# Performance work log

Hardware: AMD Instinct MI355X
Metric: run time of the kernel (lower is better)

The kernel has to match this reference:

```python
import jax, jax.numpy as jnp
import numpy as np

P_TOKENS = 200  # num_prompt_tokens
N_HEADS = 4


def setup_inputs() -> dict:
    key = jax.random.key(0)
    ks = jax.random.split(key, 6)
    B, N, C = 64, 1224, 1024
    D = 256  # bottleneck / down_size
    s = 0.02
    return {
        "x": jax.random.normal(ks[0], (B, N, C), dtype=jnp.float32),
        "down_W": jax.random.normal(ks[1], (D, C), dtype=jnp.float32) * s,
        "down_b": jnp.zeros((D,), jnp.float32),
        "up_W": jax.random.normal(ks[2], (C, D), dtype=jnp.float32) * s,
        "up_b": jnp.zeros((C,), jnp.float32),
        "in_proj_W": jax.random.normal(ks[3], (3 * D, D), dtype=jnp.float32) * s,
        "in_proj_b": jnp.zeros((3 * D,), jnp.float32),
        "out_proj_W": jax.random.normal(ks[4], (D, D), dtype=jnp.float32) * s,
        "out_proj_b": jnp.zeros((D,), jnp.float32),
        "gate": jnp.float32(1.0),
    }


def _forward(x, down_W, down_b, up_W, up_b, in_proj_W, in_proj_b,
             out_proj_W, out_proj_b, gate):
    B, N, C = x.shape
    E = down_W.shape[0]
    hd = E // N_HEADS
    # down projection + exact GELU (torch nn.GELU default)
    down = jax.nn.gelu(x @ down_W.T + down_b, approximate=False)  # [B,N,E]
    prompt = down[:, :P_TOKENS, :]   # [B,P,E]
    tok = down[:, P_TOKENS:, :]      # [B,T,E]
    # --- nn.MultiheadAttention(prompt, prompt, prompt) ---
    qkv = prompt @ in_proj_W.T + in_proj_b            # [B,P,3E]
    q, k, v = jnp.split(qkv, 3, axis=-1)
    def heads(t):
        return t.reshape(B, P_TOKENS, N_HEADS, hd)
    q, k, v = heads(q), heads(k), heads(v)
    attn = jnp.einsum('bqhd,bkhd->bhqk', q, k) / jnp.sqrt(jnp.float32(hd))
    attn = jax.nn.softmax(attn, axis=-1)
    sa = jnp.einsum('bhqk,bkhd->bqhd', attn, v).reshape(B, P_TOKENS, E)
    sa = sa @ out_proj_W.T + out_proj_b               # [B,P,E]
    # --- manual cross attention prompt -> tokens ---
    scale = jnp.float32(E) ** -0.5
    cross = jax.nn.softmax(jnp.einsum('bpe,bte->bpt', sa, tok) * scale, axis=-1)
    prompt_out = jnp.einsum('bpt,bte->bpe', cross, tok)  # [B,P,E]
    combined = jnp.concatenate([prompt_out, tok], axis=1)  # [B,N,E]
    up = combined @ up_W.T + up_b                          # [B,N,C]
    return gate * up


def reference(x, down_W, down_b, up_W, up_b, in_proj_W, in_proj_b,
              out_proj_W, out_proj_b, gate):
    return _forward(x, down_W, down_b, up_W, up_b, in_proj_W, in_proj_b,
                    out_proj_W, out_proj_b, gate)
```

## Files before the change

kernel.cpp:

```cpp
#include <hip/hip_runtime.h>
#include <math.h>

#define BB 64
#define NN 1224
#define CC 1024
#define DD 256
#define PP 200
#define TT 1024
#define HH 4
#define HDD 64

typedef __attribute__((ext_vector_type(8))) short bf16x8;
typedef __attribute__((ext_vector_type(4))) float f32x4;
typedef unsigned short u16;
typedef unsigned long long u64;

__device__ __forceinline__ u16 f2bf(float f) {
  union { float f; unsigned int u; } v; v.f = f;
  unsigned int r = v.u + 0x7FFF + ((v.u >> 16) & 1);
  return (u16)(r >> 16);
}
__device__ __forceinline__ float bf2f(u16 h) {
  union { unsigned int u; float f; } v; v.u = ((unsigned int)h) << 16;
  return v.f;
}
__device__ __forceinline__ unsigned int pk2(float a, float b) {
  return (unsigned int)f2bf(a) | ((unsigned int)f2bf(b) << 16);
}
__device__ __forceinline__ void gload16(const void* g, void* l) {
  __builtin_amdgcn_global_load_lds(
      (const __attribute__((address_space(1))) void*)g,
      (__attribute__((address_space(3))) void*)l, 16, 0, 0);
}
__device__ __forceinline__ f32x4 ntld4(const float* p) {
  return __builtin_nontemporal_load((const f32x4*)p);
}

static const size_t SZ_DOWN = (size_t)BB * NN * DD * 2;
static const size_t SZ_TOKT = (size_t)BB * DD * TT * 2;
static const size_t SZ_Q    = (size_t)BB * HH * PP * HDD * 2;
static const size_t SZ_SCORES = (size_t)BB * PP * TT * 2;

static const size_t B_DOWN   = 0;
static const size_t B_TOKT   = B_DOWN + SZ_DOWN;
static const size_t B_POOL   = B_TOKT + SZ_TOKT;
static const size_t B_QB     = B_POOL;
static const size_t B_KB     = B_QB + SZ_Q;
static const size_t B_VB     = B_KB + SZ_Q;
static const size_t B_SA     = B_VB + SZ_Q;
static const size_t B_SA2    = B_SA + SZ_Q;
static const size_t B_PBF    = B_POOL;
static const size_t B_POUTBF = B_SA2;
static const size_t B_SCORES = B_SA2 + SZ_Q;
static const size_t B_W      = B_SCORES + SZ_SCORES * 2;
static const size_t B_WD     = B_W;
static const size_t B_WU     = B_WD + 524288;
static const size_t B_WIP    = B_WU + 524288;
static const size_t B_WOP    = B_WIP + 393216;

#define MFMA_STEP64(Ab, Bb) \
  _Pragma("unroll") \
  for (int kk = 0; kk < 64; kk += 32) { \
    bf16x8 af[4], bfr[2]; \
    _Pragma("unroll") \
    for (int mi = 0; mi < 4; ++mi) { \
      const int R = mi * 16 + (lane & 15); \
      const int byt = (R * 128 + (kk + (lane >> 4) * 8) * 2) ^ ((R & 7) << 4); \
      af[mi] = *(const bf16x8*)((const char*)Ab + byt); \
    } \
    _Pragma("unroll") \
    for (int ni = 0; ni < 2; ++ni) { \
      const int R = wave * 32 + ni * 16 + (lane & 15); \
      const int byt = (R * 128 + (kk + (lane >> 4) * 8) * 2) ^ ((R & 7) << 4); \
      bfr[ni] = *(const bf16x8*)((const char*)Bb + byt); \
    } \
    _Pragma("unroll") \
    for (int mi = 0; mi < 4; ++mi) \
      _Pragma("unroll") \
      for (int ni = 0; ni < 2; ++ni) \
        acc[mi][ni] = __builtin_amdgcn_mfma_f32_16x16x32_bf16(af[mi], bfr[ni], acc[mi][ni], 0, 0, 0); \
  }

#define GLOAD_A1(Ab, SRC) \
  { \
    const int L = wave * 1024 + lane * 16; \
    const int r = L >> 7; \
    const int ce = ((L & 127) ^ ((r & 7) << 4)) >> 1; \
    gload16((SRC), (char*)Ab + wave * 1024); \
  }

#define GLOAD_B4(Bb, SRC) \
  _Pragma("unroll") \
  for (int ii = 0; ii < 4; ++ii) { \
    const int slot = wave * 4 + ii; \
    const int L = slot * 1024 + lane * 16; \
    const int r = L >> 7; \
    const int ce = ((L & 127) ^ ((r & 7) << 4)) >> 1; \
    gload16((SRC), (char*)Bb + slot * 1024); \
  }

#define PIPE_WAIT(N) asm volatile("s_waitcnt vmcnt(" #N ")" ::: "memory");
#define PIPE_BAR() \
  __builtin_amdgcn_s_barrier(); \
  __builtin_amdgcn_sched_barrier(0);
#define PIPE_END() \
  asm volatile("s_waitcnt lgkmcnt(0)" ::: "memory"); \
  __builtin_amdgcn_s_barrier(); \
  __builtin_amdgcn_sched_barrier(0);

__global__ __launch_bounds__(256) void k_castw(const float* __restrict__ dW,
                                               const float* __restrict__ uW,
                                               const float* __restrict__ iW,
                                               const float* __restrict__ oW,
                                               u16* __restrict__ dWb, u16* __restrict__ uWb,
                                               u16* __restrict__ iWb, u16* __restrict__ oWb)
{
  const int id = blockIdx.x * 256 + threadIdx.x;
  const float* s; u16* d; int off;
  if (id < 65536)       { s = dW; d = dWb; off = id; }
  else if (id < 131072) { s = uW; d = uWb; off = id - 65536; }
  else if (id < 180224) { s = iW; d = iWb; off = id - 131072; }
  else                  { s = oW; d = oWb; off = id - 180224; }
  const float4 v = ((const float4*)s)[off];
  uint2 p; p.x = pk2(v.x, v.y); p.y = pk2(v.z, v.w);
  *(uint2*)&d[(size_t)off * 4] = p;
}

__global__ __launch_bounds__(512) void k_down(const float* __restrict__ x,
                                              const u16* __restrict__ Wd,
                                              const float* __restrict__ bias,
                                              u16* __restrict__ out,
                                              u16* __restrict__ tokT)
{
  __shared__ u16 Ab[2][64 * 64];
  __shared__ u16 Bb[2][256 * 64];
  const int tid = threadIdx.x;
  const int lane = tid & 63, wave = tid >> 6;
  f32x4 acc[4][2] = {};
  const int m0 = blockIdx.x * 64;
  const int ar0 = tid >> 4;
  const int c4 = (tid & 15) * 4;

  f32x4 areg[2];
#pragma unroll
  for (int i = 0; i < 2; ++i)
    areg[i] = ntld4(&x[(size_t)(m0 + ar0 + 32 * i) * CC + c4]);
#pragma unroll
  for (int i = 0; i < 2; ++i) {
    const int r = ar0 + 32 * i;
    uint2 p; p.x = pk2(areg[i].x, areg[i].y); p.y = pk2(areg[i].z, areg[i].w);
    *(uint2*)((char*)Ab[0] + ((r * 128 + c4 * 2) ^ ((r & 7) << 4))) = p;
  }
  GLOAD_B4(Bb[0], &Wd[(size_t)r * CC + 0 + ce])
#pragma unroll
  for (int i = 0; i < 2; ++i)
    areg[i] = ntld4(&x[(size_t)(m0 + ar0 + 32 * i) * CC + 64 + c4]);

  for (int it = 0; it < 16; ++it) {
    const int cur = it & 1;
    if (it < 14) {
#pragma unroll
      for (int i = 0; i < 2; ++i) {
        const int r = ar0 + 32 * i;
        uint2 p; p.x = pk2(areg[i].x, areg[i].y); p.y = pk2(areg[i].z, areg[i].w);
        *(uint2*)((char*)Ab[cur ^ 1] + ((r * 128 + c4 * 2) ^ ((r & 7) << 4))) = p;
      }
      const int kx = (it + 2) * 64;
#pragma unroll
      for (int i = 0; i < 2; ++i)
        areg[i] = ntld4(&x[(size_t)(m0 + ar0 + 32 * i) * CC + kx + c4]);
      const int kb = (it + 1) * 64;
      GLOAD_B4(Bb[cur ^ 1], &Wd[(size_t)r * CC + kb + ce])
      asm volatile("s_waitcnt vmcnt(6) lgkmcnt(0)" ::: "memory");
    } else if (it == 14) {
#pragma unroll
      for (int i = 0; i < 2; ++i) {
        const int r = ar0 + 32 * i;
        uint2 p; p.x = pk2(areg[i].x, areg[i].y); p.y = pk2(areg[i].z, areg[i].w);
        *(uint2*)((char*)Ab[cur ^ 1] + ((r * 128 + c4 * 2) ^ ((r & 7) << 4))) = p;
      }
      GLOAD_B4(Bb[cur ^ 1], &Wd[(size_t)r * CC + 960 + ce])
      asm volatile("s_waitcnt vmcnt(4) lgkmcnt(0)" ::: "memory");
    } else {
      asm volatile("s_waitcnt vmcnt(0) lgkmcnt(0)" ::: "memory");
    }
    PIPE_BAR()
    MFMA_STEP64(Ab[cur], Bb[cur])
    PIPE_END()
  }
#pragma unroll
  for (int mi = 0; mi < 4; ++mi) {
#pragma unroll
    for (int ni = 0; ni < 2; ++ni) {
      const int col = wave * 32 + ni * 16 + (lane & 15);
      const float bv = bias[col];
      u16 vs[4];
#pragma unroll
      for (int r = 0; r < 4; ++r) {
        const int row = m0 + mi * 16 + (lane >> 4) * 4 + r;
        float v = acc[mi][ni][r] + bv;
        v = 0.5f * v * (1.f + erff(v * 0.7071067811865475f));
        vs[r] = f2bf(v);
        out[(size_t)row * DD + col] = vs[r];
      }
      const int row0 = m0 + mi * 16 + (lane >> 4) * 4;
      const int b = row0 / NN, rr = row0 - b * NN;
      if (rr >= PP) {
        const u64 pk = (u64)vs[0] | ((u64)vs[1] << 16) | ((u64)vs[2] << 32) | ((u64)vs[3] << 48);
        *(u64*)&tokT[((size_t)(b * DD + col)) * TT + (rr - PP)] = pk;
      }
    }
  }
}

__global__ __launch_bounds__(512) void k_qkv(const u16* __restrict__ down,
                                             const u16* __restrict__ Wip,
                                             const float* __restrict__ bias,
                                             u16* __restrict__ qb,
                                             u16* __restrict__ kb,
                                             u16* __restrict__ vb)
{
  __shared__ u16 Ab[2][64 * 64];
  __shared__ u16 Bb[2][256 * 64];
  const int tid = threadIdx.x;
  const int lane = tid & 63, wave = tid >> 6;
  f32x4 acc[4][2] = {};
  const int m0 = blockIdx.x * 64;
  const int nt = blockIdx.y;

#define QKV_A(BUF, K0) GLOAD_A1(BUF, ({ const int m = m0 + r; const int b = m / PP; const int p = m - b * PP; \
                    &down[((size_t)(b * NN + p)) * DD + (K0) + ce]; }))
  QKV_A(Ab[0], 0)
  GLOAD_B4(Bb[0], &Wip[(size_t)(nt * 256 + r) * DD + 0 + ce])
  for (int it = 0; it < 4; ++it) {
    const int cur = it & 1;
    if (it < 3) {
      const int k0 = (it + 1) * 64;
      QKV_A(Ab[cur ^ 1], k0)
      GLOAD_B4(Bb[cur ^ 1], &Wip[(size_t)(nt * 256 + r) * DD + k0 + ce])
      PIPE_WAIT(5)
    } else { PIPE_WAIT(0) }
    PIPE_BAR()
    MFMA_STEP64(Ab[cur], Bb[cur])
    PIPE_END()
  }
#undef QKV_A
  u16* dst = (nt == 0) ? qb : ((nt == 1) ? kb : vb);
#pragma unroll
  for (int mi = 0; mi < 4; ++mi) {
#pragma unroll
    for (int ni = 0; ni < 2; ++ni) {
      const int n = wave * 32 + ni * 16 + (lane & 15);
      const float bv = bias[nt * 256 + n];
      const int h = n >> 6, dd = n & 63;
#pragma unroll
      for (int r = 0; r < 4; ++r) {
        const int m = m0 + mi * 16 + (lane >> 4) * 4 + r;
        const int b = m / PP, p = m - b * PP;
        dst[(((size_t)(b * HH + h)) * PP + p) * HDD + dd] = f2bf(acc[mi][ni][r] + bv);
      }
    }
  }
}

__global__ __launch_bounds__(512) void k_attn(const u16* __restrict__ qb,
                                              const u16* __restrict__ kb,
                                              const u16* __restrict__ vb,
                                              u16* __restrict__ sa)
{
  __shared__ u16 Ks[208 * 64];
  __shared__ u16 Vt[64 * 232];
  __shared__ u16 Pb[8 * 16 * 232];
  const int tid = threadIdx.x, lane = tid & 63, wave = tid >> 6;
  const int bh = blockIdx.x;
  const size_t kvbase = (size_t)bh * (PP * HDD);

  for (int it = 0; it < 7; ++it) {
    const int idx = tid + 512 * it;
    if (idx < 3200) {
      const int e = idx * 4;
      const int j = e >> 6, d = e & 63;
      const u64 kv = *(const u64*)&kb[kvbase + e];
      const int byt = (j * 128 + d * 2) ^ ((j & 7) << 4);
      *(u64*)((char*)Ks + byt) = kv;
      const u64 vv = *(const u64*)&vb[kvbase + e];
      const u16* vp = (const u16*)&vv;
#pragma unroll
      for (int w = 0; w < 4; ++w) Vt[(d + w) * 232 + j] = vp[w];
    }
  }
  if (tid < 128) {
    const int rr = 200 + (tid >> 4), c = (tid & 15) * 4;
    const int byt = (rr * 128 + c * 2) ^ ((rr & 7) << 4);
    *(u64*)((char*)Ks + byt) = 0ULL;
  }
  {
    const int d = tid >> 3, cg = tid & 7;
    *(u64*)&Vt[d * 232 + 200 + cg * 4] = 0ULL;
  }
  {
    u16* pw = Pb + wave * (16 * 232);
#pragma unroll
    for (int w = 0; w < 2; ++w) {
      const int idx = lane + 64 * w;
      if (idx < 96) {
        const int row = idx / 6, cg = idx - row * 6;
        *(u64*)&pw[row * 232 + 208 + cg * 4] = 0ULL;
      }
    }
  }
  __syncthreads();

  const int b_ = bh >> 2, h = bh & 3;
  const u16* qbase = qb + kvbase;
  u16* pw = Pb + wave * (16 * 232);

  for (int f = wave; f < 13; f += 8) {
    int qrow = f * 16 + (lane & 15); if (qrow > 199) qrow = 199;
    bf16x8 qa[2];
#pragma unroll
    for (int kk = 0; kk < 2; ++kk)
      qa[kk] = *(const bf16x8*)&qbase[(size_t)qrow * 64 + kk * 32 + (lane >> 4) * 8];

    f32x4 s[13];
#pragma unroll
    for (int nf = 0; nf < 13; ++nf) {
      const int R = nf * 16 + (lane & 15);
      f32x4 a = {};
#pragma unroll
      for (int kk = 0; kk < 2; ++kk) {
        const int byt = (R * 128 + (kk * 32 + (lane >> 4) * 8) * 2) ^ ((R & 7) << 4);
        const bf16x8 kf = *(const bf16x8*)((const char*)Ks + byt);
        a = __builtin_amdgcn_mfma_f32_16x16x32_bf16(qa[kk], kf, a, 0, 0, 0);
      }
      s[nf] = a;
    }
    float mx[4] = {-1e30f, -1e30f, -1e30f, -1e30f};
#pragma unroll
    for (int nf = 0; nf < 13; ++nf) {
      const int col = nf * 16 + (lane & 15);
#pragma unroll
      for (int r = 0; r < 4; ++r) {
        float v = (col < PP) ? s[nf][r] * 0.125f : -INFINITY;
        s[nf][r] = v;
        mx[r] = fmaxf(mx[r], v);
      }
    }
#pragma unroll
    for (int off = 1; off < 16; off <<= 1)
#pragma unroll
      for (int r = 0; r < 4; ++r) mx[r] = fmaxf(mx[r], __shfl_xor(mx[r], off));
    float sum[4] = {0.f, 0.f, 0.f, 0.f};
#pragma unroll
    for (int nf = 0; nf < 13; ++nf)
#pragma unroll
      for (int r = 0; r < 4; ++r) {
        const float e = expf(s[nf][r] - mx[r]);
        s[nf][r] = e;
        sum[r] += e;
      }
#pragma unroll
    for (int off = 1; off < 16; off <<= 1)
#pragma unroll
      for (int r = 0; r < 4; ++r) sum[r] += __shfl_xor(sum[r], off);
    float inv[4];
#pragma unroll
    for (int r = 0; r < 4; ++r) inv[r] = 1.f / sum[r];
#pragma unroll
    for (int nf = 0; nf < 13; ++nf) {
      const int col = nf * 16 + (lane & 15);
#pragma unroll
      for (int r = 0; r < 4; ++r) {
        const int row = (lane >> 4) * 4 + r;
        pw[row * 232 + col] = f2bf(s[nf][r] * inv[r]);
      }
    }
    f32x4 o[4] = {};
#pragma unroll
    for (int kk = 0; kk < 7; ++kk) {
      const bf16x8 pa = *(const bf16x8*)((const char*)pw +
                         ((lane & 15) * 232 + kk * 32 + (lane >> 4) * 8) * 2);
#pragma unroll
      for (int nf4 = 0; nf4 < 4; ++nf4) {
        const bf16x8 vv = *(const bf16x8*)((const char*)Vt +
                           (((lane & 15) + 16 * nf4) * 232 + kk * 32 + (lane >> 4) * 8) * 2);
        o[nf4] = __builtin_amdgcn_mfma_f32_16x16x32_bf16(pa, vv, o[nf4], 0, 0, 0);
      }
    }
#pragma unroll
    for (int nf4 = 0; nf4 < 4; ++nf4) {
      const int d = (lane & 15) + 16 * nf4;
#pragma unroll
      for (int r = 0; r < 4; ++r) {
        const int p = f * 16 + (lane >> 4) * 4 + r;
        if (p < PP)
          sa[((size_t)(b_ * PP + p)) * DD + h * HDD + d] = f2bf(o[nf4][r]);
      }
    }
  }
}

__global__ __launch_bounds__(512) void k_oproj(const u16* __restrict__ A,
                                               const u16* __restrict__ Wop,
                                               const float* __restrict__ bias,
                                               u16* __restrict__ out)
{
  __shared__ u16 Ab[2][64 * 64];
  __shared__ u16 Bb[2][256 * 64];
  const int tid = threadIdx.x;
  const int lane = tid & 63, wave = tid >> 6;
  f32x4 acc[4][2] = {};
  const int m0 = blockIdx.x * 64;

  GLOAD_A1(Ab[0], &A[(size_t)(m0 + r) * DD + 0 + ce])
  GLOAD_B4(Bb[0], &Wop[(size_t)r * DD + 0 + ce])
  for (int it = 0; it < 4; ++it) {
    const int cur = it & 1;
    if (it < 3) {
      const int k0 = (it + 1) * 64;
      GLOAD_A1(Ab[cur ^ 1], &A[(size_t)(m0 + r) * DD + k0 + ce])
      GLOAD_B4(Bb[cur ^ 1], &Wop[(size_t)r * DD + k0 + ce])
      PIPE_WAIT(5)
    } else { PIPE_WAIT(0) }
    PIPE_BAR()
    MFMA_STEP64(Ab[cur], Bb[cur])
    PIPE_END()
  }
#pragma unroll
  for (int mi = 0; mi < 4; ++mi) {
#pragma unroll
    for (int ni = 0; ni < 2; ++ni) {
      const int col = wave * 32 + ni * 16 + (lane & 15);
      const float bv = bias[col];
#pragma unroll
      for (int r = 0; r < 4; ++r) {
        const int row = m0 + mi * 16 + (lane >> 4) * 4 + r;
        out[(size_t)row * DD + col] = f2bf(acc[mi][ni][r] + bv);
      }
    }
  }
}

__global__ __launch_bounds__(512) void k_scores(const u16* __restrict__ sa2,
                                                const u16* __restrict__ down,
                                                u16* __restrict__ scores)
{
  __shared__ u16 Ab[2][64 * 64];
  __shared__ u16 Bb[2][256 * 64];
  const int tid = threadIdx.x;
  const int lane = tid & 63, wave = tid >> 6;
  f32x4 acc[4][2] = {};
  const int b = blockIdx.x, mh = blockIdx.y, nt = blockIdx.z;

#define SC_A(BUF, K0) GLOAD_A1(BUF, ({ int p = mh * 64 + r; p = (p < PP) ? p : (PP - 1); \
                    &sa2[((size_t)(b * PP + p)) * DD + (K0) + ce]; }))
  SC_A(Ab[0], 0)
  GLOAD_B4(Bb[0], &down[((size_t)(b * NN + PP + nt * 256 + r)) * DD + 0 + ce])
  for (int it = 0; it < 4; ++it) {
    const int cur = it & 1;
    if (it < 3) {
      const int k0 = (it + 1) * 64;
      SC_A(Ab[cur ^ 1], k0)
      GLOAD_B4(Bb[cur ^ 1], &down[((size_t)(b * NN + PP + nt * 256 + r)) * DD + k0 + ce])
      PIPE_WAIT(5)
    } else { PIPE_WAIT(0) }
    PIPE_BAR()
    MFMA_STEP64(Ab[cur], Bb[cur])
    PIPE_END()
  }
#undef SC_A
#pragma unroll
  for (int mi = 0; mi < 4; ++mi) {
#pragma unroll
    for (int ni = 0; ni < 2; ++ni) {
      const int t = nt * 256 + wave * 32 + ni * 16 + (lane & 15);
#pragma unroll
      for (int r = 0; r < 4; ++r) {
        const int p = mh * 64 + mi * 16 + (lane >> 4) * 4 + r;
        if (p < PP)
          scores[((size_t)(b * PP + p)) * TT + t] = f2bf(acc[mi][ni][r] * 0.0625f);
      }
    }
  }
}

__global__ __launch_bounds__(256) void k_softmax(const u16* __restrict__ s,
                                                 u16* __restrict__ pbf)
{
  const int row = blockIdx.x;
  const int t = threadIdx.x;
  const int lane = t & 63, w = t >> 6;
  __shared__ float red[4];
  const u64 raw = *(const u64*)&s[(size_t)row * TT + t * 4];
  float v[4];
#pragma unroll
  for (int i = 0; i < 4; ++i) v[i] = bf2f((u16)(raw >> (16 * i)));
  float mx = fmaxf(fmaxf(v[0], v[1]), fmaxf(v[2], v[3]));
#pragma unroll
  for (int off = 32; off; off >>= 1) mx = fmaxf(mx, __shfl_xor(mx, off));
  if (lane == 0) red[w] = mx;
  __syncthreads();
  mx = fmaxf(fmaxf(red[0], red[1]), fmaxf(red[2], red[3]));
  __syncthreads();
  float sum = 0.f;
#pragma unroll
  for (int i = 0; i < 4; ++i) { v[i] = expf(v[i] - mx); sum += v[i]; }
#pragma unroll
  for (int off = 32; off; off >>= 1) sum += __shfl_xor(sum, off);
  if (lane == 0) red[w] = sum;
  __syncthreads();
  sum = red[0] + red[1] + red[2] + red[3];
  const float inv = 1.f / sum;
  u64 pk = (u64)f2bf(v[0] * inv) | ((u64)f2bf(v[1] * inv) << 16) |
           ((u64)f2bf(v[2] * inv) << 32) | ((u64)f2bf(v[3] * inv) << 48);
  *(u64*)&pbf[(size_t)row * TT + t * 4] = pk;
}

__global__ __launch_bounds__(512) void k_pout(const u16* __restrict__ pbf,
                                              const u16* __restrict__ tokT,
                                              u16* __restrict__ out)
{
  __shared__ u16 Ab[2][64 * 64];
  __shared__ u16 Bb[2][256 * 64];
  const int tid = threadIdx.x;
  const int lane = tid & 63, wave = tid >> 6;
  f32x4 acc[4][2] = {};
  const int b = blockIdx.x, mh = blockIdx.y;

#define PO_A(BUF, K0) GLOAD_A1(BUF, ({ int p = mh * 64 + r; p = (p < PP) ? p : (PP - 1); \
                    &pbf[((size_t)(b * PP + p)) * TT + (K0) + ce]; }))
  PO_A(Ab[0], 0)
  GLOAD_B4(Bb[0], &tokT[((size_t)(b * DD + r)) * TT + 0 + ce])
  for (int it = 0; it < 16; ++it) {
    const int cur = it & 1;
    if (it < 15) {
      const int k0 = (it + 1) * 64;
      PO_A(Ab[cur ^ 1], k0)
      GLOAD_B4(Bb[cur ^ 1], &tokT[((size_t)(b * DD + r)) * TT + k0 + ce])
      PIPE_WAIT(5)
    } else { PIPE_WAIT(0) }
    PIPE_BAR()
    MFMA_STEP64(Ab[cur], Bb[cur])
    PIPE_END()
  }
#undef PO_A
#pragma unroll
  for (int mi = 0; mi < 4; ++mi) {
#pragma unroll
    for (int ni = 0; ni < 2; ++ni) {
      const int e = wave * 32 + ni * 16 + (lane & 15);
#pragma unroll
      for (int r = 0; r < 4; ++r) {
        const int p = mh * 64 + mi * 16 + (lane >> 4) * 4 + r;
        if (p < PP)
          out[((size_t)(b * PP + p)) * DD + e] = f2bf(acc[mi][ni][r]);
      }
    }
  }
}

__global__ __launch_bounds__(512) void k_up(const u16* __restrict__ poutbf,
                                            const u16* __restrict__ down,
                                            const u16* __restrict__ Wu,
                                            const float* __restrict__ bias,
                                            const float* __restrict__ gate,
                                            float* __restrict__ out)
{
  __shared__ u16 Ab[2][64 * 64];
  __shared__ u16 Bb[2][256 * 64];
  const int tid = threadIdx.x;
  const int lane = tid & 63, wave = tid >> 6;
  f32x4 acc[4][2] = {};
  const int m0 = blockIdx.x * 64;
  const int n0 = blockIdx.y * 256;

#define UP_A(BUF, K0) GLOAD_A1(BUF, ({ const int m = m0 + r; const int b = m / NN; const int rr = m - b * NN; \
                     const u16* base = (rr < PP) ? &poutbf[((size_t)(b * PP + rr)) * DD] \
                                                 : &down[((size_t)(b * NN + rr)) * DD]; \
                     base + (K0) + ce; }))
  UP_A(Ab[0], 0)
  GLOAD_B4(Bb[0], &Wu[(size_t)(n0 + r) * DD + 0 + ce])
  for (int it = 0; it < 4; ++it) {
    const int cur = it & 1;
    if (it < 3) {
      const int k0 = (it + 1) * 64;
      UP_A(Ab[cur ^ 1], k0)
      GLOAD_B4(Bb[cur ^ 1], &Wu[(size_t)(n0 + r) * DD + k0 + ce])
      PIPE_WAIT(5)
    } else { PIPE_WAIT(0) }
    PIPE_BAR()
    MFMA_STEP64(Ab[cur], Bb[cur])
    PIPE_END()
  }
#undef UP_A
  const float g = gate[0];
#pragma unroll
  for (int mi = 0; mi < 4; ++mi) {
#pragma unroll
    for (int ni = 0; ni < 2; ++ni) {
      const int col = n0 + wave * 32 + ni * 16 + (lane & 15);
      const float bv = bias[col];
#pragma unroll
      for (int r = 0; r < 4; ++r) {
        const int row = m0 + mi * 16 + (lane >> 4) * 4 + r;
        __builtin_nontemporal_store((acc[mi][ni][r] + bv) * g, &out[(size_t)row * CC + col]);
      }
    }
  }
}

extern "C" void kernel_launch(void* const* d_in, const int* in_sizes, int n_in,
                              void* d_out, int out_size, void* d_ws, size_t ws_size,
                              hipStream_t stream) {
  const float* x          = (const float*)d_in[0];
  const float* down_W     = (const float*)d_in[1];
  const float* down_b     = (const float*)d_in[2];
  const float* up_W       = (const float*)d_in[3];
  const float* up_b       = (const float*)d_in[4];
  const float* in_proj_W  = (const float*)d_in[5];
  const float* in_proj_b  = (const float*)d_in[6];
  const float* out_proj_W = (const float*)d_in[7];
  const float* out_proj_b = (const float*)d_in[8];
  const float* gate       = (const float*)d_in[9];
  float* out = (float*)d_out;

  char* wsb = (char*)d_ws;
  u16* down_bf = (u16*)(wsb + B_DOWN);
  u16* tokT    = (u16*)(wsb + B_TOKT);
  u16* qb      = (u16*)(wsb + B_QB);
  u16* kb      = (u16*)(wsb + B_KB);
  u16* vb      = (u16*)(wsb + B_VB);
  u16* sa_bf   = (u16*)(wsb + B_SA);
  u16* sa2_bf  = (u16*)(wsb + B_SA2);
  u16* pbf     = (u16*)(wsb + B_PBF);
  u16* poutbf  = (u16*)(wsb + B_POUTBF);
  u16* scores  = (u16*)(wsb + B_SCORES);
  u16* Wd  = (u16*)(wsb + B_WD);
  u16* Wu  = (u16*)(wsb + B_WU);
  u16* Wip = (u16*)(wsb + B_WIP);
  u16* Wop = (u16*)(wsb + B_WOP);

  k_castw<<<dim3(768), 256, 0, stream>>>(down_W, up_W, in_proj_W, out_proj_W, Wd, Wu, Wip, Wop);
  k_down<<<dim3((BB * NN) / 64), 512, 0, stream>>>(x, Wd, down_b, down_bf, tokT);
  k_qkv<<<dim3(200, 3), 512, 0, stream>>>(down_bf, Wip, in_proj_b, qb, kb, vb);
  k_attn<<<dim3(BB * HH), 512, 0, stream>>>(qb, kb, vb, sa_bf);
  k_oproj<<<dim3(200), 512, 0, stream>>>(sa_bf, Wop, out_proj_b, sa2_bf);
  k_scores<<<dim3(BB, 4, 4), 512, 0, stream>>>(sa2_bf, down_bf, scores);
  k_softmax<<<dim3(BB * PP), 256, 0, stream>>>(scores, pbf);
  k_pout<<<dim3(BB, 4), 512, 0, stream>>>(pbf, tokT, poutbf);
  k_up<<<dim3((BB * NN) / 64, CC / 256), 512, 0, stream>>>(poutbf, down_bf, Wu, up_b, gate, out);
}
```

Baseline: 309.7 us.

## Fuse out-projection, cross-attention scores and softmax into one kernel

Merges k_oproj, k_scores and k_softmax into a single k_fuse kernel per (batch, 64-prompt-row) tile. The projected prompt tile stays in shared memory and the full 64x1024 score row block is held in registers, so softmax runs in place without writing and re-reading the bf16 score buffer. This removes two launches and the score round trip through global memory. The cost is fewer blocks (256 instead of 1024 for scores) and heavy register use for 128 accumulator floats per thread, which may limit occupancy.

```diff
diff --git a/kernel.cpp b/kernel.cpp
--- a/kernel.cpp
+++ b/kernel.cpp
@@ -49,9 +49,9 @@
 static const size_t B_VB     = B_KB + SZ_Q;
 static const size_t B_SA     = B_VB + SZ_Q;
 static const size_t B_SA2    = B_SA + SZ_Q;
-static const size_t B_PBF    = B_POOL;
 static const size_t B_POUTBF = B_SA2;
 static const size_t B_SCORES = B_SA2 + SZ_Q;
+static const size_t B_PBF    = B_SCORES;
 static const size_t B_W      = B_SCORES + SZ_SCORES * 2;
 static const size_t B_WD     = B_W;
 static const size_t B_WU     = B_WD + 524288;
@@ -81,6 +81,29 @@
         acc[mi][ni] = __builtin_amdgcn_mfma_f32_16x16x32_bf16(af[mi], bfr[ni], acc[mi][ni], 0, 0, 0); \
   }
 
+#define MFMA_AF(SACC, K0, Bbuf) \
+  _Pragma("unroll") \
+  for (int kk = 0; kk < 64; kk += 32) { \
+    bf16x8 af[4], bfr[2]; \
+    _Pragma("unroll") \
+    for (int mi = 0; mi < 4; ++mi) { \
+      const int R = mi * 16 + (lane & 15); \
+      const int byt = (R * 512 + ((K0) + kk + (lane >> 4) * 8) * 2) ^ ((R & 7) << 4); \
+      af[mi] = *(const bf16x8*)((const char*)Afull + byt); \
+    } \
+    _Pragma("unroll") \
+    for (int ni = 0; ni < 2; ++ni) { \
+      const int R = wave * 32 + ni * 16 + (lane & 15); \
+      const int byt = (R * 128 + (kk + (lane >> 4) * 8) * 2) ^ ((R & 7) << 4); \
+      bfr[ni] = *(const bf16x8*)((const char*)Bbuf + byt); \
+    } \
+    _Pragma("unroll") \
+    for (int mi = 0; mi < 4; ++mi) \
+      _Pragma("unroll") \
+      for (int ni = 0; ni < 2; ++ni) \
+        SACC[mi][ni] = __builtin_amdgcn_mfma_f32_16x16x32_bf16(af[mi], bfr[ni], SACC[mi][ni], 0, 0, 0); \
+  }
+
 #define GLOAD_A1(Ab, SRC) \
   { \
     const int L = wave * 1024 + lane * 16; \
@@ -400,25 +423,32 @@
   }
 }
 
-__global__ __launch_bounds__(512) void k_oproj(const u16* __restrict__ A,
-                                               const u16* __restrict__ Wop,
-                                               const float* __restrict__ bias,
-                                               u16* __restrict__ out)
+__global__ __launch_bounds__(512, 2) void k_fuse(const u16* __restrict__ A,
+                                                 const u16* __restrict__ Wop,
+                                                 const float* __restrict__ bias,
+                                                 const u16* __restrict__ down,
+                                                 u16* __restrict__ pbf)
 {
   __shared__ u16 Ab[2][64 * 64];
   __shared__ u16 Bb[2][256 * 64];
+  __shared__ u16 Afull[64 * 256];
+  __shared__ float Mred[8][64];
+  __shared__ float Lred[8][64];
   const int tid = threadIdx.x;
   const int lane = tid & 63, wave = tid >> 6;
+  const int b = blockIdx.x, mh = blockIdx.y;
+  const int m0 = mh * 64;
+
   f32x4 acc[4][2] = {};
-  const int m0 = blockIdx.x * 64;
-
-  GLOAD_A1(Ab[0], &A[(size_t)(m0 + r) * DD + 0 + ce])
+#define FU_A(BUF, K0) GLOAD_A1(BUF, ({ int p = m0 + r; p = (p < PP) ? p : (PP - 1); \
+                    &A[((size_t)(b * PP + p)) * DD + (K0) + ce]; }))
+  FU_A(Ab[0], 0)
   GLOAD_B4(Bb[0], &Wop[(size_t)r * DD + 0 + ce])
   for (int it = 0; it < 4; ++it) {
     const int cur = it & 1;
     if (it < 3) {
       const int k0 = (it + 1) * 64;
-      GLOAD_A1(Ab[cur ^ 1], &A[(size_t)(m0 + r) * DD + k0 + ce])
+      FU_A(Ab[cur ^ 1], k0)
       GLOAD_B4(Bb[cur ^ 1], &Wop[(size_t)r * DD + k0 + ce])
       PIPE_WAIT(5)
     } else { PIPE_WAIT(0) }
@@ -426,6 +456,10 @@
     MFMA_STEP64(Ab[cur], Bb[cur])
     PIPE_END()
   }
+#undef FU_A
+
+  GLOAD_B4(Bb[0], &down[((size_t)(b * NN + PP + r)) * DD + 0 + ce])
+
 #pragma unroll
   for (int mi = 0; mi < 4; ++mi) {
 #pragma unroll
@@ -434,86 +468,131 @@
       const float bv = bias[col];
 #pragma unroll
       for (int r = 0; r < 4; ++r) {
-        const int row = m0 + mi * 16 + (lane >> 4) * 4 + r;
-        out[(size_t)row * DD + col] = f2bf(acc[mi][ni][r] + bv);
-      }
-    }
-  }
-}
-
-__global__ __launch_bounds__(512) void k_scores(const u16* __restrict__ sa2,
-                                                const u16* __restrict__ down,
-                                                u16* __restrict__ scores)
-{
-  __shared__ u16 Ab[2][64 * 64];
-  __shared__ u16 Bb[2][256 * 64];
-  const int tid = threadIdx.x;
-  const int lane = tid & 63, wave = tid >> 6;
-  f32x4 acc[4][2] = {};
-  const int b = blockIdx.x, mh = blockIdx.y, nt = blockIdx.z;
-
-#define SC_A(BUF, K0) GLOAD_A1(BUF, ({ int p = mh * 64 + r; p = (p < PP) ? p : (PP - 1); \
-                    &sa2[((size_t)(b * PP + p)) * DD + (K0) + ce]; }))
-  SC_A(Ab[0], 0)
-  GLOAD_B4(Bb[0], &down[((size_t)(b * NN + PP + nt * 256 + r)) * DD + 0 + ce])
-  for (int it = 0; it < 4; ++it) {
-    const int cur = it & 1;
-    if (it < 3) {
-      const int k0 = (it + 1) * 64;
-      SC_A(Ab[cur ^ 1], k0)
-      GLOAD_B4(Bb[cur ^ 1], &down[((size_t)(b * NN + PP + nt * 256 + r)) * DD + k0 + ce])
-      PIPE_WAIT(5)
+        const int row = mi * 16 + (lane >> 4) * 4 + r;
+        *(u16*)((char*)Afull + ((row * 512 + col * 2) ^ ((row & 7) << 4))) =
+            f2bf(acc[mi][ni][r] + bv);
+      }
+    }
+  }
+  __syncthreads();
+
+  f32x4 s4[4][4][2] = {};
+#pragma unroll
+  for (int st = 0; st < 16; ++st) {
+    const int cur = st & 1;
+    if (st < 15) {
+      const int nx = st + 1;
+      const int nt2 = nx >> 2, k02 = (nx & 3) * 64;
+      GLOAD_B4(Bb[cur ^ 1], &down[((size_t)(b * NN + PP + nt2 * 256 + r)) * DD + k02 + ce])
+      PIPE_WAIT(4)
     } else { PIPE_WAIT(0) }
     PIPE_BAR()
-    MFMA_STEP64(Ab[cur], Bb[cur])
+    {
+      const int k0s = (st & 3) * 64;
+      MFMA_AF(s4[st >> 2], k0s, Bb[cur])
+    }
     PIPE_END()
   }
-#undef SC_A
-#pragma unroll
-  for (int mi = 0; mi < 4; ++mi) {
-#pragma unroll
-    for (int ni = 0; ni < 2; ++ni) {
-      const int t = nt * 256 + wave * 32 + ni * 16 + (lane & 15);
-#pragma unroll
-      for (int r = 0; r < 4; ++r) {
-        const int p = mh * 64 + mi * 16 + (lane >> 4) * 4 + r;
-        if (p < PP)
-          scores[((size_t)(b * PP + p)) * TT + t] = f2bf(acc[mi][ni][r] * 0.0625f);
-      }
-    }
-  }
-}
-
-__global__ __launch_bounds__(256) void k_softmax(const u16* __restrict__ s,
-                                                 u16* __restrict__ pbf)
-{
-  const int row = blockIdx.x;
-  const int t = threadIdx.x;
-  const int lane = t & 63, w = t >> 6;
-  __shared__ float red[4];
-  const u64 raw = *(const u64*)&s[(size_t)row * TT + t * 4];
-  float v[4];
-#pragma unroll
-  for (int i = 0; i < 4; ++i) v[i] = bf2f((u16)(raw >> (16 * i)));
-  float mx = fmaxf(fmaxf(v[0], v[1]), fmaxf(v[2], v[3]));
-#pragma unroll
-  for (int off = 32; off; off >>= 1) mx = fmaxf(mx, __shfl_xor(mx, off));
-  if (lane == 0) red[w] = mx;
+
+  float mx[4][4];
+#pragma unroll
+  for (int mi = 0; mi < 4; ++mi)
+#pragma unroll
+    for (int r = 0; r < 4; ++r) mx[mi][r] = -1e30f;
+#pragma unroll
+  for (int nt = 0; nt < 4; ++nt)
+#pragma unroll
+    for (int mi = 0; mi < 4; ++mi)
+#pragma unroll
+      for (int ni = 0; ni < 2; ++ni)
+#pragma unroll
+        for (int r = 0; r < 4; ++r) {
+          const float v = s4[nt][mi][ni][r] * 0.0625f;
+          s4[nt][mi][ni][r] = v;
+          mx[mi][r] = fmaxf(mx[mi][r], v);
+        }
+#pragma unroll
+  for (int off = 1; off < 16; off <<= 1)
+#pragma unroll
+    for (int mi = 0; mi < 4; ++mi)
+#pragma unroll
+      for (int r = 0; r < 4; ++r) mx[mi][r] = fmaxf(mx[mi][r], __shfl_xor(mx[mi][r], off));
+  if ((lane & 15) == 0) {
+#pragma unroll
+    for (int mi = 0; mi < 4; ++mi)
+#pragma unroll
+      for (int r = 0; r < 4; ++r)
+        Mred[wave][mi * 16 + (lane >> 4) * 4 + r] = mx[mi][r];
+  }
   __syncthreads();
-  mx = fmaxf(fmaxf(red[0], red[1]), fmaxf(red[2], red[3]));
+  float M[4][4];
+#pragma unroll
+  for (int mi = 0; mi < 4; ++mi)
+#pragma unroll
+    for (int r = 0; r < 4; ++r) {
+      const int row = mi * 16 + (lane >> 4) * 4 + r;
+      float m = Mred[0][row];
+#pragma unroll
+      for (int w = 1; w < 8; ++w) m = fmaxf(m, Mred[w][row]);
+      M[mi][r] = m;
+    }
+  float l[4][4];
+#pragma unroll
+  for (int mi = 0; mi < 4; ++mi)
+#pragma unroll
+    for (int r = 0; r < 4; ++r) l[mi][r] = 0.f;
+#pragma unroll
+  for (int nt = 0; nt < 4; ++nt)
+#pragma unroll
+    for (int mi = 0; mi < 4; ++mi)
+#pragma unroll
+      for (int ni = 0; ni < 2; ++ni)
+#pragma unroll
+        for (int r = 0; r < 4; ++r) {
+          const float e = __expf(s4[nt][mi][ni][r] - M[mi][r]);
+          s4[nt][mi][ni][r] = e;
+          l[mi][r] += e;
+        }
+#pragma unroll
+  for (int off = 1; off < 16; off <<= 1)
+#pragma unroll
+    for (int mi = 0; mi < 4; ++mi)
+#pragma unroll
+      for (int r = 0; r < 4; ++r) l[mi][r] += __shfl_xor(l[mi][r], off);
+  if ((lane & 15) == 0) {
+#pragma unroll
+    for (int mi = 0; mi < 4; ++mi)
+#pragma unroll
+      for (int r = 0; r < 4; ++r)
+        Lred[wave][mi * 16 + (lane >> 4) * 4 + r] = l[mi][r];
+  }
   __syncthreads();
-  float sum = 0.f;
-#pragma unroll
-  for (int i = 0; i < 4; ++i) { v[i] = expf(v[i] - mx); sum += v[i]; }
-#pragma unroll
-  for (int off = 32; off; off >>= 1) sum += __shfl_xor(sum, off);
-  if (lane == 0) red[w] = sum;
-  __syncthreads();
-  sum = red[0] + red[1] + red[2] + red[3];
-  const float inv = 1.f / sum;
-  u64 pk = (u64)f2bf(v[0] * inv) | ((u64)f2bf(v[1] * inv) << 16) |
-           ((u64)f2bf(v[2] * inv) << 32) | ((u64)f2bf(v[3] * inv) << 48);
-  *(u64*)&pbf[(size_t)row * TT + t * 4] = pk;
+  float inv[4][4];
+#pragma unroll
+  for (int mi = 0; mi < 4; ++mi)
+#pragma unroll
+    for (int r = 0; r < 4; ++r) {
+      const int row = mi * 16 + (lane >> 4) * 4 + r;
+      float t = 0.f;
+#pragma unroll
+      for (int w = 0; w < 8; ++w) t += Lred[w][row];
+      inv[mi][r] = 1.f / t;
+    }
+
+#pragma unroll
+  for (int nt = 0; nt < 4; ++nt)
+#pragma unroll
+    for (int mi = 0; mi < 4; ++mi)
+#pragma unroll
+      for (int ni = 0; ni < 2; ++ni) {
+        const int t = nt * 256 + wave * 32 + ni * 16 + (lane & 15);
+#pragma unroll
+        for (int r = 0; r < 4; ++r) {
+          const int p = m0 + mi * 16 + (lane >> 4) * 4 + r;
+          if (p < PP)
+            pbf[((size_t)(b * PP + p)) * TT + t] = f2bf(s4[nt][mi][ni][r] * inv[mi][r]);
+        }
+      }
 }
 
 __global__ __launch_bounds__(512) void k_pout(const u16* __restrict__ pbf,
@@ -631,10 +710,8 @@
   u16* kb      = (u16*)(wsb + B_KB);
   u16* vb      = (u16*)(wsb + B_VB);
   u16* sa_bf   = (u16*)(wsb + B_SA);
-  u16* sa2_bf  = (u16*)(wsb + B_SA2);
   u16* pbf     = (u16*)(wsb + B_PBF);
   u16* poutbf  = (u16*)(wsb + B_POUTBF);
-  u16* scores  = (u16*)(wsb + B_SCORES);
   u16* Wd  = (u16*)(wsb + B_WD);
   u16* Wu  = (u16*)(wsb + B_WU);
   u16* Wip = (u16*)(wsb + B_WIP);
@@ -644,9 +721,7 @@
   k_down<<<dim3((BB * NN) / 64), 512, 0, stream>>>(x, Wd, down_b, down_bf, tokT);
   k_qkv<<<dim3(200, 3), 512, 0, stream>>>(down_bf, Wip, in_proj_b, qb, kb, vb);
   k_attn<<<dim3(BB * HH), 512, 0, stream>>>(qb, kb, vb, sa_bf);
-  k_oproj<<<dim3(200), 512, 0, stream>>>(sa_bf, Wop, out_proj_b, sa2_bf);
-  k_scores<<<dim3(BB, 4, 4), 512, 0, stream>>>(sa2_bf, down_bf, scores);
-  k_softmax<<<dim3(BB * PP), 256, 0, stream>>>(scores, pbf);
+  k_fuse<<<dim3(BB, 4), 512, 0, stream>>>(sa_bf, Wop, out_proj_b, down_bf, pbf);
   k_pout<<<dim3(BB, 4), 512, 0, stream>>>(pbf, tokT, poutbf);
   k_up<<<dim3((BB * NN) / 64, CC / 256), 512, 0, stream>>>(poutbf, down_bf, Wu, up_b, gate, out);
 }
```

New measurement: 306.0 us. Within noise of the previous version (-1.2%).
